# Optimization experiments

Measured on AMD Instinct MI355X. Metric: run time of the kernel, lower is better.

The kernel has to match this reference:

```python
import jax, jax.numpy as jnp
import numpy as np

# ViT-Small config
L, D, H, HD = 12, 384, 6, 64
P, IMG, NCLS = 16, 224, 1000
NPATCH = (IMG // P) ** 2  # 196
GAMMA, MIN_TOKENS, EPS = 0.5, 16, 1e-6
SCALE = HD ** -0.5


def _ln(x, w, b, eps=1e-6):
    mu = jnp.mean(x, axis=-1, keepdims=True)
    var = jnp.var(x, axis=-1, keepdims=True)
    return (x - mu) * jax.lax.rsqrt(var + eps) * w + b


def _qkv_split(xn, w, b):
    # xn: [B, Nt, D] -> q,k,v each [B, H, Nt, HD]
    B, Nt, _ = xn.shape
    qkv = (xn @ w.T + b).reshape(B, Nt, 3, H, HD).transpose(2, 0, 3, 1, 4)
    return qkv[0], qkv[1], qkv[2]


def _vit_forward(x, patch_w, patch_b, cls_token, pos_embed,
                 ln1_w, ln1_b, qkv_w, qkv_b, proj_w, proj_b,
                 ln2_w, ln2_b, fc1_w, fc1_b, fc2_w, fc2_b,
                 norm_w, norm_b, head_w, head_b, keep_schedule=None):
    B = x.shape[0]
    # patch embed: conv stride 16 -> [B, D, 14, 14] -> [B, 196, D]
    xp = jax.lax.conv_general_dilated(x, patch_w, (P, P), 'VALID',
                                      dimension_numbers=('NCHW', 'OIHW', 'NCHW'))
    xp = xp.reshape(B, D, NPATCH).transpose(0, 2, 1) + patch_b
    cls = jnp.broadcast_to(cls_token, (B, 1, D))
    xt = jnp.concatenate([cls, xp], axis=1) + pos_embed  # [B, 197, D]

    N = NPATCH
    prev_mass = jnp.asarray(1.0, jnp.float32)
    schedule = []
    for l in range(L):
        if keep_schedule is not None:
            keep_idx = keep_schedule[l]
        elif N > MIN_TOKENS:
            # CLS-only attention importance scoring (cheap pass)
            xn = _ln(xt, ln1_w[l], ln1_b[l])
            q, k, v = _qkv_split(xn, qkv_w[l], qkv_b[l])
            a_cls = jax.nn.softmax(jnp.einsum('bhqd,bhkd->bhqk', q[:, :, :1], k) * SCALE, axis=-1)[:, :, 0, :]  # [B,H,Nt]
            vnorm = jnp.linalg.norm(v, axis=-1)  # [B,H,Nt]
            imp = (a_cls * vnorm).mean(axis=1)   # [B,Nt]
            imp_p = imp[:, 1:]                   # patch importance
            mass = jnp.mean(imp_p.sum(-1) / (imp.sum(-1) + EPS))
            keep_ratio = float(jnp.clip(GAMMA * mass / (prev_mass + EPS), 0.0, 1.0))
            N_next = max(MIN_TOKENS, int(N * keep_ratio))
            if N_next < N:
                scores = imp_p.mean(0)  # shared keep set across batch (index_select semantics)
                top = jax.lax.top_k(scores, N_next)[1]
                keep_idx = jnp.concatenate([jnp.zeros((1,), jnp.int32),
                                            jnp.sort(top).astype(jnp.int32) + 1])
            else:
                keep_idx = None
            prev_mass = mass
        else:
            keep_idx = None
        schedule.append(keep_idx)
        if keep_idx is not None:
            xt = jnp.take(xt, keep_idx, axis=1)
            N = int(keep_idx.shape[0]) - 1

        # full transformer block on surviving tokens
        Nt = xt.shape[1]
        xn = _ln(xt, ln1_w[l], ln1_b[l])
        q, k, v = _qkv_split(xn, qkv_w[l], qkv_b[l])
        a = jax.nn.softmax(jnp.einsum('bhqd,bhkd->bhqk', q, k) * SCALE, axis=-1)
        o = jnp.einsum('bhqk,bhkd->bhqd', a, v).transpose(0, 2, 1, 3).reshape(B, Nt, D)
        xt = xt + o @ proj_w[l].T + proj_b[l]
        h = _ln(xt, ln2_w[l], ln2_b[l])
        h = jax.nn.gelu(h @ fc1_w[l].T + fc1_b[l], approximate=False)
        xt = xt + h @ fc2_w[l].T + fc2_b[l]

    xt = _ln(xt, norm_w, norm_b)
    logits = xt[:, 0] @ head_w.T + head_b
    return logits, schedule


def setup_inputs() -> dict:
    key = jax.random.key(0)
    ks = jax.random.split(key, 10)
    rn = lambda k, s, sc=0.02: jax.random.normal(k, s, jnp.float32) * sc
    return {
        'x': jax.random.normal(ks[0], (64, 3, IMG, IMG), jnp.float32),
        'patch_w': rn(ks[1], (D, 3, P, P)),
        'patch_b': jnp.zeros((D,), jnp.float32),
        'cls_token': rn(ks[2], (1, 1, D)),
        'pos_embed': rn(ks[3], (1, NPATCH + 1, D)),
        'ln1_w': jnp.ones((L, D), jnp.float32), 'ln1_b': jnp.zeros((L, D), jnp.float32),
        'qkv_w': rn(ks[4], (L, 3 * D, D)), 'qkv_b': jnp.zeros((L, 3 * D), jnp.float32),
        'proj_w': rn(ks[5], (L, D, D)), 'proj_b': jnp.zeros((L, D), jnp.float32),
        'ln2_w': jnp.ones((L, D), jnp.float32), 'ln2_b': jnp.zeros((L, D), jnp.float32),
        'fc1_w': rn(ks[6], (L, 4 * D, D)), 'fc1_b': jnp.zeros((L, 4 * D), jnp.float32),
        'fc2_w': rn(ks[7], (L, D, 4 * D)), 'fc2_b': jnp.zeros((L, D), jnp.float32),
        'norm_w': jnp.ones((D,), jnp.float32), 'norm_b': jnp.zeros((D,), jnp.float32),
        'head_w': rn(ks[8], (NCLS, D)), 'head_b': jnp.zeros((NCLS,), jnp.float32),
    }


def reference(x, patch_w, patch_b, cls_token, pos_embed, ln1_w, ln1_b, qkv_w, qkv_b,
              proj_w, proj_b, ln2_w, ln2_b, fc1_w, fc1_b, fc2_w, fc2_b,
              norm_w, norm_b, head_w, head_b):
    logits, _ = _vit_forward(x, patch_w, patch_b, cls_token, pos_embed, ln1_w, ln1_b,
                             qkv_w, qkv_b, proj_w, proj_b, ln2_w, ln2_b,
                             fc1_w, fc1_b, fc2_w, fc2_b, norm_w, norm_b, head_w, head_b)
    return logits
```

## Files before the change

kernel.cpp:

```cpp
#include <hip/hip_runtime.h>
#include <hip/hip_bf16.h>

static constexpr int kL = 12;
static constexpr int kD = 384;
static constexpr int kH = 6;
static constexpr int kB = 64;
static constexpr int kNP = 196;
static constexpr int kBAND = 197;
static constexpr int kNCLS = 1000;
static constexpr float kSCALE = 0.125f;
static constexpr float kEPS = 1e-6f;
static constexpr size_t kWQ = (size_t)kB * kH * kBAND * 64;
static constexpr int kBH = kB * kH;

typedef __attribute__((ext_vector_type(8))) short short8;
typedef __attribute__((ext_vector_type(4))) float f32x4;

__device__ __forceinline__ float gelu_f(float x) {
    return 0.5f * x * (1.0f + erff(x * 0.70710678118654752440f));
}
__device__ __forceinline__ unsigned short f2bf(float x) {
    __hip_bfloat16 h = __float2bfloat16(x);
    return *(unsigned short*)&h;
}
__device__ __forceinline__ float bf2f(unsigned short u) {
    unsigned int x = ((unsigned int)u) << 16;
    return __uint_as_float(x);
}

__global__ __launch_bounds__(384) void k_init(int* si, float* sf,
                                              const float* __restrict__ cls,
                                              const float* __restrict__ pos,
                                              unsigned short* __restrict__ xtA,
                                              float2* __restrict__ pstats) {
    int b = blockIdx.x, c = threadIdx.x;
    unsigned short hv = f2bf(cls[c] + pos[c]);
    xtA[(size_t)b * kBAND * kD + c] = hv;
    float v = bf2f(hv);
    __shared__ float r1[384], r2[384];
    r1[c] = v; r2[c] = v * v;
    __syncthreads();
    if (c < 128) { r1[c] += r1[c + 128] + r1[c + 256]; r2[c] += r2[c + 128] + r2[c + 256]; }
    __syncthreads();
    for (int st = 64; st; st >>= 1) {
        if (c < st) { r1[c] += r1[c + st]; r2[c] += r2[c + st]; }
        __syncthreads();
    }
    if (c == 0) {
        pstats[(size_t)(b * kBAND) * 8 + 0] = make_float2(r1[0], r2[0]);
#pragma unroll
        for (int nn = 1; nn < 6; ++nn) pstats[(size_t)(b * kBAND) * 8 + nn] = make_float2(0.f, 0.f);
        if (b == 0) { si[0] = kBAND; sf[0] = 1.0f; }
    }
}

__global__ __launch_bounds__(256) void k_cvtall(
    const float* __restrict__ s0, const float* __restrict__ s1, const float* __restrict__ s2,
    const float* __restrict__ s3, const float* __restrict__ s4,
    __hip_bfloat16* __restrict__ d0, __hip_bfloat16* __restrict__ d1, __hip_bfloat16* __restrict__ d2,
    __hip_bfloat16* __restrict__ d3, __hip_bfloat16* __restrict__ d4) {
    const int c0 = 73728, c1 = 1400832, c2 = 1843200, c3 = 3612672, c4 = 5382144;
    int stride = gridDim.x * 256;
    for (int i = blockIdx.x * 256 + threadIdx.x; i < c4; i += stride) {
        const float* src; __hip_bfloat16* dst; int off;
        if (i < c0)      { src = s0; dst = d0; off = i; }
        else if (i < c1) { src = s1; dst = d1; off = i - c0; }
        else if (i < c2) { src = s2; dst = d2; off = i - c1; }
        else if (i < c3) { src = s3; dst = d3; off = i - c2; }
        else             { src = s4; dst = d4; off = i - c3; }
        float4 v = ((const float4*)src)[off];
        dst[4 * off + 0] = __float2bfloat16(v.x);
        dst[4 * off + 1] = __float2bfloat16(v.y);
        dst[4 * off + 2] = __float2bfloat16(v.z);
        dst[4 * off + 3] = __float2bfloat16(v.w);
    }
}

template<int ACT_GELU, int MODE, int LNA, int STATS>
__global__ __launch_bounds__(256) void k_mgemm(
    const void* __restrict__ Av, int lda,
    const unsigned short* __restrict__ W, int K,
    const float* __restrict__ bias,
    unsigned short* __restrict__ Cv, int ldc,
    const void* __restrict__ Rv,
    const int* __restrict__ keepR,
    const float* __restrict__ lnw, const float* __restrict__ lnb,
    int rT, int nT, int band,
    const int* __restrict__ NtPtr, int ntConst,
    const float2* __restrict__ pstatsIn, float2* __restrict__ pstatsOut)
{
    __shared__ __align__(16) unsigned char pool[18432];
    unsigned short (*As)[72] = (unsigned short (*)[72])pool;
    unsigned short (*Ws)[72] = (unsigned short (*)[72])(pool + 9216);
    unsigned short (*Cu)[76] = (unsigned short (*)[76])pool;
    __shared__ float mus[64], rss[64];

    int Nt = NtPtr ? NtPtr[0] : ntConst;
    unsigned int rowsTotal = (unsigned int)kB * (unsigned int)Nt;

    int L = blockIdx.x;
    int xcd = L & 7;
    int m = L >> 3;
    int n = m % nT;
    int r = (m / nT) * 8 + xcd;
    if (r >= rT) return;
    unsigned int r0 = (unsigned int)r * 64;
    int n0 = n * 64;
    if (r0 >= rowsTotal) return;

    const float* Rf = (const float*)Rv;
    const unsigned short* Rb = (const unsigned short*)Rv;

    int tid = threadIdx.x;
    int srow = tid >> 3;
    int scol = (tid & 7) << 3;

    unsigned int rv0 = r0 + srow, rv1 = r0 + srow + 32;
    bool v0 = rv0 < rowsTotal, v1 = rv1 < rowsTotal;
    const unsigned short* ah0 = nullptr; const unsigned short* ah1 = nullptr;
    const float* xb0 = nullptr; const float* xb1 = nullptr;
    if (MODE == 2) {
        if (v0) {
            unsigned int bb = rv0 / (unsigned int)Nt, tt = rv0 - bb * Nt;
            int py = tt / 14, px = tt - py * 14;
            xb0 = (const float*)Av + (size_t)bb * 3 * 224 * 224 + (py * 16) * 224 + px * 16;
        }
        if (v1) {
            unsigned int bb = rv1 / (unsigned int)Nt, tt = rv1 - bb * Nt;
            int py = tt / 14, px = tt - py * 14;
            xb1 = (const float*)Av + (size_t)bb * 3 * 224 * 224 + (py * 16) * 224 + px * 16;
        }
    } else {
        if (v0) {
            unsigned int bb = rv0 / (unsigned int)Nt, tt = rv0 - bb * Nt;
            ah0 = (const unsigned short*)Av + ((size_t)bb * band + tt) * lda;
        }
        if (v1) {
            unsigned int bb = rv1 / (unsigned int)Nt, tt = rv1 - bb * Nt;
            ah1 = (const unsigned short*)Av + ((size_t)bb * band + tt) * lda;
        }
    }
    const unsigned short* wp0 = W + (size_t)(n0 + srow) * K;
    const unsigned short* wp1 = W + (size_t)(n0 + srow + 32) * K;

    float mu0 = 0.f, rs0 = 0.f, mu1 = 0.f, rs1 = 0.f;
    if (LNA) {
        if (tid < 64) {
            unsigned int rv = r0 + tid;
            float mu = 0.f, rsd = 0.f;
            if (rv < rowsTotal) {
                unsigned int bb = rv / (unsigned int)Nt, tt = rv - bb * Nt;
                const float2* ps = pstatsIn + ((size_t)bb * band + tt) * 8;
                float s1 = 0.f, s2 = 0.f;
#pragma unroll
                for (int nn = 0; nn < 6; ++nn) { float2 p = ps[nn]; s1 += p.x; s2 += p.y; }
                mu = s1 * (1.f / 384.f);
                float var = fmaxf(s2 * (1.f / 384.f) - mu * mu, 0.f);
                rsd = rsqrtf(var + kEPS);
            }
            mus[tid] = mu; rss[tid] = rsd;
        }
        __syncthreads();
        mu0 = mus[srow]; rs0 = rss[srow];
        mu1 = mus[srow + 32]; rs1 = rss[srow + 32];
    }

    int wave = tid >> 6, lane = tid & 63;
    int wr32 = ((wave >> 1) & 1) * 32, wc32 = (wave & 1) * 32;
    int l15 = lane & 15, l4 = lane >> 4;

    f32x4 acc00 = {}, acc01 = {}, acc10 = {}, acc11 = {};

    for (int k0 = 0; k0 < K; k0 += 64) {
        uint4 zero = make_uint4(0, 0, 0, 0);
        uint4 a0 = zero, a1 = zero;
        uint4 w0 = *(const uint4*)(wp0 + k0 + scol);
        uint4 w1 = *(const uint4*)(wp1 + k0 + scol);
        if (MODE == 2) {
            int k = k0 + scol;
            int c = k >> 8;
            int rr_ = k & 255;
            int ky = rr_ >> 4, kx = rr_ & 15;
            size_t off = (size_t)c * 50176 + (size_t)ky * 224 + kx;
            if (v0) {
                float4 x0 = *(const float4*)(xb0 + off);
                float4 x1 = *(const float4*)(xb0 + off + 4);
                unsigned short p[8];
                p[0] = f2bf(x0.x); p[1] = f2bf(x0.y); p[2] = f2bf(x0.z); p[3] = f2bf(x0.w);
                p[4] = f2bf(x1.x); p[5] = f2bf(x1.y); p[6] = f2bf(x1.z); p[7] = f2bf(x1.w);
                a0 = *(uint4*)p;
            }
            if (v1) {
                float4 x0 = *(const float4*)(xb1 + off);
                float4 x1 = *(const float4*)(xb1 + off + 4);
                unsigned short p[8];
                p[0] = f2bf(x0.x); p[1] = f2bf(x0.y); p[2] = f2bf(x0.z); p[3] = f2bf(x0.w);
                p[4] = f2bf(x1.x); p[5] = f2bf(x1.y); p[6] = f2bf(x1.z); p[7] = f2bf(x1.w);
                a1 = *(uint4*)p;
            }
        } else if (LNA) {
            float4 lw0 = *(const float4*)(lnw + k0 + scol);
            float4 lw1 = *(const float4*)(lnw + k0 + scol + 4);
            float4 lb0 = *(const float4*)(lnb + k0 + scol);
            float4 lb1 = *(const float4*)(lnb + k0 + scol + 4);
            if (v0) {
                uint4 raw = *(const uint4*)(ah0 + k0 + scol);
                const unsigned short* u = (const unsigned short*)&raw;
                unsigned short p[8];
                p[0] = f2bf((bf2f(u[0]) - mu0) * rs0 * lw0.x + lb0.x);
                p[1] = f2bf((bf2f(u[1]) - mu0) * rs0 * lw0.y + lb0.y);
                p[2] = f2bf((bf2f(u[2]) - mu0) * rs0 * lw0.z + lb0.z);
                p[3] = f2bf((bf2f(u[3]) - mu0) * rs0 * lw0.w + lb0.w);
                p[4] = f2bf((bf2f(u[4]) - mu0) * rs0 * lw1.x + lb1.x);
                p[5] = f2bf((bf2f(u[5]) - mu0) * rs0 * lw1.y + lb1.y);
                p[6] = f2bf((bf2f(u[6]) - mu0) * rs0 * lw1.z + lb1.z);
                p[7] = f2bf((bf2f(u[7]) - mu0) * rs0 * lw1.w + lb1.w);
                a0 = *(uint4*)p;
            }
            if (v1) {
                uint4 raw = *(const uint4*)(ah1 + k0 + scol);
                const unsigned short* u = (const unsigned short*)&raw;
                unsigned short p[8];
                p[0] = f2bf((bf2f(u[0]) - mu1) * rs1 * lw0.x + lb0.x);
                p[1] = f2bf((bf2f(u[1]) - mu1) * rs1 * lw0.y + lb0.y);
                p[2] = f2bf((bf2f(u[2]) - mu1) * rs1 * lw0.z + lb0.z);
                p[3] = f2bf((bf2f(u[3]) - mu1) * rs1 * lw0.w + lb0.w);
                p[4] = f2bf((bf2f(u[4]) - mu1) * rs1 * lw1.x + lb1.x);
                p[5] = f2bf((bf2f(u[5]) - mu1) * rs1 * lw1.y + lb1.y);
                p[6] = f2bf((bf2f(u[6]) - mu1) * rs1 * lw1.z + lb1.z);
                p[7] = f2bf((bf2f(u[7]) - mu1) * rs1 * lw1.w + lb1.w);
                a1 = *(uint4*)p;
            }
        } else {
            a0 = v0 ? *(const uint4*)(ah0 + k0 + scol) : zero;
            a1 = v1 ? *(const uint4*)(ah1 + k0 + scol) : zero;
        }
        __syncthreads();
        *(uint4*)&As[srow][scol] = a0;
        *(uint4*)&As[srow + 32][scol] = a1;
        *(uint4*)&Ws[srow][scol] = w0;
        *(uint4*)&Ws[srow + 32][scol] = w1;
        __syncthreads();
#pragma unroll
        for (int ks = 0; ks < 2; ++ks) {
            short8 af_0 = *(const short8*)&As[wr32 + l15][ks * 32 + l4 * 8];
            short8 af_1 = *(const short8*)&As[wr32 + 16 + l15][ks * 32 + l4 * 8];
            short8 bf_0 = *(const short8*)&Ws[wc32 + l15][ks * 32 + l4 * 8];
            short8 bf_1 = *(const short8*)&Ws[wc32 + 16 + l15][ks * 32 + l4 * 8];
            acc00 = __builtin_amdgcn_mfma_f32_16x16x32_bf16(af_0, bf_0, acc00, 0, 0, 0);
            acc01 = __builtin_amdgcn_mfma_f32_16x16x32_bf16(af_0, bf_1, acc01, 0, 0, 0);
            acc10 = __builtin_amdgcn_mfma_f32_16x16x32_bf16(af_1, bf_0, acc10, 0, 0, 0);
            acc11 = __builtin_amdgcn_mfma_f32_16x16x32_bf16(af_1, bf_1, acc11, 0, 0, 0);
        }
    }

    __syncthreads();
    f32x4 accs[2][2] = { { acc00, acc01 }, { acc10, acc11 } };
#pragma unroll
    for (int fi = 0; fi < 2; ++fi) {
        int lrow = wr32 + fi * 16 + l4 * 4;
        unsigned int rvb = r0 + lrow;
#pragma unroll
        for (int fj = 0; fj < 2; ++fj) {
            int lcol = wc32 + fj * 16 + l15;
            float bv = bias ? bias[n0 + lcol] : 0.f;
#pragma unroll
            for (int rr = 0; rr < 4; ++rr) {
                unsigned int rv = rvb + rr;
                float v = accs[fi][fj][rr] + bv;
                if (ACT_GELU) v = gelu_f(v);
                if (MODE == 2) {
                    if (rv < rowsTotal) {
                        unsigned int bb = rv / (unsigned int)Nt;
                        unsigned int tt = rv - bb * (unsigned int)Nt;
                        v += Rf[(size_t)(tt + 1) * kD + n0 + lcol];
                    }
                } else if (Rv && rv < rowsTotal) {
                    unsigned int bb = rv / (unsigned int)Nt;
                    unsigned int tt = rv - bb * (unsigned int)Nt;
                    size_t rrow = keepR ? ((size_t)bb * band + keepR[tt]) : ((size_t)bb * band + tt);
                    v += bf2f(Rb[rrow * ldc + n0 + lcol]);
                }
                Cu[lrow + rr][lcol] = f2bf(v);
            }
        }
    }
    __syncthreads();

#pragma unroll
    for (int i = 0; i < 2; ++i) {
        int id = tid + (i << 8);
        int row = id >> 3, c2 = id & 7;
        unsigned int rv = r0 + row;
        if (rv < rowsTotal) {
            unsigned int bb = rv / (unsigned int)Nt;
            unsigned int tt = rv - bb * (unsigned int)Nt;
            uint4 val = *(const uint4*)&Cu[row][c2 << 3];
            if (MODE == 1) {
                int which = n0 >= 768 ? 2 : (n0 >= 384 ? 1 : 0);
                int hh = (n0 - which * 384) >> 6;
                *(uint4*)(Cv + (size_t)which * kWQ +
                          (((size_t)bb * kH + hh) * kBAND + tt) * 64 + ((n0 & 63) + (c2 << 3))) = val;
            } else if (MODE == 2) {
                *(uint4*)(Cv + ((size_t)bb * kBAND + tt + 1) * ldc + n0 + (c2 << 3)) = val;
            } else {
                *(uint4*)(Cv + ((size_t)bb * band + tt) * ldc + n0 + (c2 << 3)) = val;
            }
            if (STATS) {
                const unsigned short* u = (const unsigned short*)&val;
                float s1 = 0.f, s2 = 0.f;
#pragma unroll
                for (int e = 0; e < 8; ++e) { float f = bf2f(u[e]); s1 += f; s2 += f * f; }
#pragma unroll
                for (int off = 1; off < 8; off <<= 1) {
                    s1 += __shfl_xor(s1, off, 64);
                    s2 += __shfl_xor(s2, off, 64);
                }
                if (c2 == 0) {
                    size_t sridx = (MODE == 2) ? ((size_t)bb * kBAND + tt + 1)
                                               : ((size_t)bb * band + tt);
                    pstatsOut[sridx * 8 + n] = make_float2(s1, s2);
                }
            }
        }
    }
}

__global__ __launch_bounds__(256) void k_decA(const __hip_bfloat16* __restrict__ qsplit,
                                              float* __restrict__ imph, float* __restrict__ sabh,
                                              const int* __restrict__ si) {
    int Nt = si[0];
    if (Nt - 1 <= 16) return;
    int tid = threadIdx.x, w = tid >> 6, lane = tid & 63;
    int bh = blockIdx.x;
    __shared__ float qs[64];
    __shared__ float sdot[224], svn[224];
    __shared__ float red[256];
    const __hip_bfloat16* qp = qsplit + (size_t)bh * kBAND * 64;
    const __hip_bfloat16* kp = qsplit + kWQ + (size_t)bh * kBAND * 64;
    const __hip_bfloat16* vp = qsplit + 2 * kWQ + (size_t)bh * kBAND * 64;
    if (tid < 64) qs[tid] = __bfloat162float(qp[tid]);
    __syncthreads();
    float qv = qs[lane];
    for (int j = w; j < Nt; j += 8) {
        int j2 = j + 4;
        bool has2 = j2 < Nt;
        float k1 = __bfloat162float(kp[(size_t)j * 64 + lane]);
        float v1 = __bfloat162float(vp[(size_t)j * 64 + lane]);
        float k2 = has2 ? __bfloat162float(kp[(size_t)j2 * 64 + lane]) : 0.f;
        float v2 = has2 ? __bfloat162float(vp[(size_t)j2 * 64 + lane]) : 0.f;
        float p1 = qv * k1, n1 = v1 * v1;
        float p2 = qv * k2, n2 = v2 * v2;
#pragma unroll
        for (int off = 1; off < 64; off <<= 1) {
            p1 += __shfl_xor(p1, off, 64); n1 += __shfl_xor(n1, off, 64);
            p2 += __shfl_xor(p2, off, 64); n2 += __shfl_xor(n2, off, 64);
        }
        if (lane == 0) {
            sdot[j] = p1 * kSCALE; svn[j] = sqrtf(n1);
            if (has2) { sdot[j2] = p2 * kSCALE; svn[j2] = sqrtf(n2); }
        }
    }
    __syncthreads();
    float s = (tid < Nt) ? sdot[tid] : -INFINITY;
    red[tid] = s; __syncthreads();
    for (int st = 128; st; st >>= 1) { if (tid < st) red[tid] = fmaxf(red[tid], red[tid + st]); __syncthreads(); }
    float mmax = red[0]; __syncthreads();
    float e = (tid < Nt) ? expf(s - mmax) : 0.f;
    red[tid] = e; __syncthreads();
    for (int st = 128; st; st >>= 1) { if (tid < st) red[tid] += red[tid + st]; __syncthreads(); }
    float inv = 1.f / red[0];
    float val = (tid < Nt) ? e * inv * svn[tid] : 0.f;
    if (tid < Nt) imph[(size_t)tid * kBH + bh] = val;
    __syncthreads();
    red[tid] = val; __syncthreads();
    for (int st = 128; st; st >>= 1) { if (tid < st) red[tid] += red[tid + st]; __syncthreads(); }
    if (tid == 0) { sabh[2 * bh] = red[0]; sabh[2 * bh + 1] = val; }
}

__global__ __launch_bounds__(256) void k_decB(int* __restrict__ si, float* __restrict__ sf,
                                              const float* __restrict__ imph,
                                              const float* __restrict__ sabh,
                                              int* __restrict__ keep) {
    int Nt = si[0];
    int tid = threadIdx.x;
    if (Nt - 1 <= 16) {
        for (int j = tid; j < Nt; j += 256) keep[j] = j;
        return;
    }
    int N = Nt - 1;
    __shared__ float red[256];
    float v = 0.f;
    if (tid < kB) {
        float sa = 0.f, i0 = 0.f;
#pragma unroll
        for (int hh = 0; hh < kH; ++hh) {
            sa += sabh[2 * (tid * kH + hh)];
            i0 += sabh[2 * (tid * kH + hh) + 1];
        }
        sa *= (1.f / 6.f); i0 *= (1.f / 6.f);
        v = (sa - i0) / (sa + kEPS);
    }
    red[tid] = v; __syncthreads();
    for (int st = 128; st; st >>= 1) { if (tid < st) red[tid] += red[tid + st]; __syncthreads(); }
    float mass = red[0] * (1.f / 64.f);
    float prev = sf[0];
    float ratio = 0.5f * mass / (prev + kEPS);
    ratio = fminf(fmaxf(ratio, 0.f), 1.f);
    int N_next = (int)((double)N * (double)ratio);
    if (N_next < 16) N_next = 16;
    if (tid == 0) sf[0] = mass;
    __syncthreads();
    if (N_next >= N) {
        for (int j = tid; j < Nt; j += 256) keep[j] = j;
        return;
    }
    __shared__ float scq[200][4];
    __shared__ float sc[200];
    __shared__ int flag[200];
    for (int task = tid; task < N * 4; task += 256) {
        int row = task >> 2, seg = task & 3;
        const float4* p = (const float4*)(imph + (size_t)(row + 1) * kBH) + seg * 24;
        float a0 = 0.f, a1 = 0.f, a2 = 0.f, a3 = 0.f;
#pragma unroll
        for (int q = 0; q < 24; q += 4) {
            float4 x0 = p[q + 0], x1 = p[q + 1], x2 = p[q + 2], x3 = p[q + 3];
            a0 += (x0.x + x0.y) + (x0.z + x0.w);
            a1 += (x1.x + x1.y) + (x1.z + x1.w);
            a2 += (x2.x + x2.y) + (x2.z + x2.w);
            a3 += (x3.x + x3.y) + (x3.z + x3.w);
        }
        scq[row][seg] = (a0 + a1) + (a2 + a3);
    }
    __syncthreads();
    if (tid < N) sc[tid] = (scq[tid][0] + scq[tid][1]) + (scq[tid][2] + scq[tid][3]);
    __syncthreads();
    if (tid < N) {
        float s2 = sc[tid];
        int rank = 0;
        for (int i = 0; i < N; ++i) {
            float o2 = sc[i];
            rank += (o2 > s2) || (o2 == s2 && i < tid);
        }
        flag[tid] = (rank < N_next) ? 1 : 0;
    }
    __syncthreads();
    if (tid == 0) {
        keep[0] = 0;
        int pos = 1;
        for (int j = 0; j < N; ++j) if (flag[j]) keep[pos++] = j + 1;
        si[0] = N_next + 1;
    }
}

__global__ __launch_bounds__(256) void k_attn2(const __hip_bfloat16* __restrict__ qsplit,
                                               __hip_bfloat16* __restrict__ o,
                                               const int* __restrict__ si,
                                               const int* __restrict__ keep) {
    __shared__ __align__(16) unsigned short Kb[224][72];
    __shared__ __align__(16) unsigned short Vt[64][228];
    __shared__ __align__(16) unsigned short Pb[4][16][228];
    int Nt = si[0];
    int bh = blockIdx.x;
    int b = bh / kH, h = bh - b * kH;
    int tid = threadIdx.x, w = tid >> 6, lane = tid & 63;
    int l15 = lane & 15, l4 = lane >> 4;
    int nJT = (Nt + 15) >> 4;
    int nKT = (Nt + 31) >> 5;
    int NTP = nKT << 5;

    const unsigned short* qb = (const unsigned short*)qsplit + (size_t)bh * kBAND * 64;
    const unsigned short* kb = (const unsigned short*)qsplit + kWQ + (size_t)bh * kBAND * 64;
    const unsigned short* vb = (const unsigned short*)qsplit + 2 * kWQ + (size_t)bh * kBAND * 64;

    {
        int rr = tid >> 3;
        int c8 = (tid & 7) << 3;
        for (int r = rr; r < NTP; r += 32) {
            uint4 kv = make_uint4(0, 0, 0, 0), vv = make_uint4(0, 0, 0, 0);
            if (r < Nt) {
                int old = keep[r];
                kv = *(const uint4*)(kb + ((size_t)old << 6) + c8);
                vv = *(const uint4*)(vb + ((size_t)old << 6) + c8);
            }
            *(uint4*)&Kb[r][c8] = kv;
            const unsigned short* vs = (const unsigned short*)&vv;
#pragma unroll
            for (int e = 0; e < 8; ++e) Vt[c8 + e][r] = vs[e];
        }
    }
    __syncthreads();

    for (int strip = w; strip < nJT; strip += 4) {
        int tq = (strip << 4) + l15;
        int told = (tq < Nt) ? keep[tq] : 0;
        const unsigned short* qrow = qb + ((size_t)told << 6) + (l4 << 3);
        short8 qf0 = *(const short8*)(qrow);
        short8 qf1 = *(const short8*)(qrow + 32);

        f32x4 sv[13];
#pragma unroll
        for (int jt = 0; jt < 13; ++jt) {
            if (jt < nJT) {
                const unsigned short* kr = &Kb[(jt << 4) + l15][l4 << 3];
                short8 kf0 = *(const short8*)(kr);
                short8 kf1 = *(const short8*)(kr + 32);
                f32x4 a = {};
                a = __builtin_amdgcn_mfma_f32_16x16x32_bf16(qf0, kf0, a, 0, 0, 0);
                a = __builtin_amdgcn_mfma_f32_16x16x32_bf16(qf1, kf1, a, 0, 0, 0);
                sv[jt] = a;
            }
        }
        float mx[4] = { -INFINITY, -INFINITY, -INFINITY, -INFINITY };
#pragma unroll
        for (int jt = 0; jt < 13; ++jt) if (jt < nJT) {
            bool ok = ((jt << 4) + l15) < Nt;
#pragma unroll
            for (int r = 0; r < 4; ++r) {
                float s = ok ? sv[jt][r] * kSCALE : -INFINITY;
                sv[jt][r] = s;
                mx[r] = fmaxf(mx[r], s);
            }
        }
#pragma unroll
        for (int r = 0; r < 4; ++r) {
            mx[r] = fmaxf(mx[r], __shfl_xor(mx[r], 1, 64));
            mx[r] = fmaxf(mx[r], __shfl_xor(mx[r], 2, 64));
            mx[r] = fmaxf(mx[r], __shfl_xor(mx[r], 4, 64));
            mx[r] = fmaxf(mx[r], __shfl_xor(mx[r], 8, 64));
        }
        float sm[4] = { 0.f, 0.f, 0.f, 0.f };
#pragma unroll
        for (int jt = 0; jt < 13; ++jt) if (jt < nJT) {
#pragma unroll
            for (int r = 0; r < 4; ++r) {
                float p = expf(sv[jt][r] - mx[r]);
                sv[jt][r] = p;
                sm[r] += p;
            }
        }
#pragma unroll
        for (int r = 0; r < 4; ++r) {
            sm[r] += __shfl_xor(sm[r], 1, 64);
            sm[r] += __shfl_xor(sm[r], 2, 64);
            sm[r] += __shfl_xor(sm[r], 4, 64);
            sm[r] += __shfl_xor(sm[r], 8, 64);
            sm[r] = 1.f / sm[r];
        }
#pragma unroll
        for (int jt = 0; jt < 13; ++jt) if (jt < nJT) {
#pragma unroll
            for (int r = 0; r < 4; ++r)
                Pb[w][(l4 << 2) + r][(jt << 4) + l15] = f2bf(sv[jt][r] * sm[r]);
        }
        for (int c = (nJT << 4) + lane; c < NTP; c += 64) {
#pragma unroll
            for (int rr2 = 0; rr2 < 16; ++rr2) Pb[w][rr2][c] = 0;
        }
        asm volatile("s_waitcnt lgkmcnt(0)" ::: "memory");
        __builtin_amdgcn_sched_barrier(0);

        f32x4 oacc[4] = { {}, {}, {}, {} };
#pragma unroll
        for (int kt = 0; kt < 7; ++kt) if (kt < nKT) {
            short8 pf = *(const short8*)&Pb[w][l15][(kt << 5) + (l4 << 3)];
#pragma unroll
            for (int dt = 0; dt < 4; ++dt) {
                short8 vf = *(const short8*)&Vt[(dt << 4) + l15][(kt << 5) + (l4 << 3)];
                oacc[dt] = __builtin_amdgcn_mfma_f32_16x16x32_bf16(pf, vf, oacc[dt], 0, 0, 0);
            }
        }
#pragma unroll
        for (int dt = 0; dt < 4; ++dt) {
#pragma unroll
            for (int r = 0; r < 4; ++r) {
                int tqo = (strip << 4) + (l4 << 2) + r;
                if (tqo < Nt)
                    o[((size_t)b * kBAND + tqo) * kD + h * 64 + (dt << 4) + l15] =
                        __float2bfloat16(oacc[dt][r]);
            }
        }
    }
}

__global__ __launch_bounds__(256) void k_head(const unsigned short* __restrict__ X,
                                              const float* __restrict__ nw, const float* __restrict__ nb,
                                              const float* __restrict__ hw, const float* __restrict__ hb,
                                              float* __restrict__ out) {
    int b = blockIdx.x >> 2;
    int tid = threadIdx.x;
    __shared__ float xs[384];
    __shared__ float red[256];
    const unsigned short* row = X + (size_t)b * kBAND * kD;
    float s1 = 0.f, s2 = 0.f;
    for (int c = tid; c < 384; c += 256) { float v = bf2f(row[c]); xs[c] = v; s1 += v; s2 += v * v; }
    red[tid] = s1; __syncthreads();
    for (int st = 128; st; st >>= 1) { if (tid < st) red[tid] += red[tid + st]; __syncthreads(); }
    float sum = red[0]; __syncthreads();
    red[tid] = s2; __syncthreads();
    for (int st = 128; st; st >>= 1) { if (tid < st) red[tid] += red[tid + st]; __syncthreads(); }
    float sq = red[0];
    float mu = sum * (1.f / 384.f);
    float var = fmaxf(sq * (1.f / 384.f) - mu * mu, 0.f);
    float rs = rsqrtf(var + kEPS);
    __syncthreads();
    for (int c = tid; c < 384; c += 256) xs[c] = (xs[c] - mu) * rs * nw[c] + nb[c];
    __syncthreads();
    int n = ((blockIdx.x & 3) << 8) + tid;
    if (n >= kNCLS) return;
    const float* wrow = hw + (size_t)n * kD;
    float acc = 0.f;
#pragma unroll 8
    for (int d = 0; d < kD; d += 4) {
        float4 w4 = *(const float4*)(wrow + d);
        acc += xs[d] * w4.x + xs[d + 1] * w4.y + xs[d + 2] * w4.z + xs[d + 3] * w4.w;
    }
    out[(size_t)b * kNCLS + n] = acc + hb[n];
}

extern "C" void kernel_launch(void* const* d_in, const int* in_sizes, int n_in,
                              void* d_out, int out_size, void* d_ws, size_t ws_size,
                              hipStream_t stream) {
    const float* x       = (const float*)d_in[0];
    const float* patch_w = (const float*)d_in[1];
    const float* patch_b = (const float*)d_in[2];
    const float* cls_tok = (const float*)d_in[3];
    const float* pos     = (const float*)d_in[4];
    const float* ln1w    = (const float*)d_in[5];
    const float* ln1b    = (const float*)d_in[6];
    const float* qkvw    = (const float*)d_in[7];
    const float* qkvb    = (const float*)d_in[8];
    const float* projw   = (const float*)d_in[9];
    const float* projb   = (const float*)d_in[10];
    const float* ln2w    = (const float*)d_in[11];
    const float* ln2b    = (const float*)d_in[12];
    const float* fc1w    = (const float*)d_in[13];
    const float* fc1b    = (const float*)d_in[14];
    const float* fc2w    = (const float*)d_in[15];
    const float* fc2b    = (const float*)d_in[16];
    const float* normw   = (const float*)d_in[17];
    const float* normb   = (const float*)d_in[18];
    const float* headw   = (const float*)d_in[19];
    const float* headb   = (const float*)d_in[20];
    float* out = (float*)d_out;

    char* ws = (char*)d_ws;
    const size_t MB = 1024ull * 1024ull;
    int*   si   = (int*)ws;
    float* sf   = (float*)(ws + 64);
    int*   keep = (int*)(ws + 256);
    float* sabh = (float*)(ws + 4096);
    float* imph = (float*)(ws + 16384);
    unsigned short* xtA = (unsigned short*)(ws + 1 * MB);
    unsigned short* xtB = (unsigned short*)(ws + 12 * MB);
    __hip_bfloat16* obuf = (__hip_bfloat16*)(ws + 23 * MB);
    __hip_bfloat16* qsplit = (__hip_bfloat16*)(ws + 33 * MB);
    __hip_bfloat16* hbuf   = (__hip_bfloat16*)(ws + 33 * MB);
    __hip_bfloat16* wpat = (__hip_bfloat16*)(ws + 110 * MB);
    __hip_bfloat16* wqkv = (__hip_bfloat16*)(ws + 111 * MB);
    __hip_bfloat16* wprj = (__hip_bfloat16*)(ws + 122 * MB);
    __hip_bfloat16* wfc1 = (__hip_bfloat16*)(ws + 126 * MB);
    __hip_bfloat16* wfc2 = (__hip_bfloat16*)(ws + 141 * MB);
    float2* pstats = (float2*)(ws + 156 * MB);

    k_init<<<64, 384, 0, stream>>>(si, sf, cls_tok, pos, xtA, pstats);
    k_cvtall<<<2048, 256, 0, stream>>>(patch_w, qkvw, projw, fc1w, fc2w,
                                       wpat, wqkv, wprj, wfc1, wfc2);

    k_mgemm<0, 2, 0, 1><<<8 * 6 * 25, 256, 0, stream>>>(
        (const void*)x, 768, (const unsigned short*)wpat, 768,
        patch_b, xtA, kD, (const void*)pos, (const int*)nullptr,
        (const float*)nullptr, (const float*)nullptr,
        196, 6, 196, (const int*)nullptr, 196,
        (const float2*)nullptr, pstats);

    unsigned short* cur = xtA; unsigned short* oth = xtB;
    for (int l = 0; l < kL; ++l) {
        const float* l1w = ln1w + l * kD;  const float* l1b = ln1b + l * kD;
        const __hip_bfloat16* qw = wqkv + (size_t)l * 1152 * kD;
        const float* qb = qkvb + l * 1152;
        const __hip_bfloat16* pw = wprj + (size_t)l * kD * kD;
        const float* pb = projb + l * kD;
        const float* l2w = ln2w + l * kD;  const float* l2b = ln2b + l * kD;
        const __hip_bfloat16* f1w = wfc1 + (size_t)l * 1536 * kD;
        const float* f1b = fc1b + l * 1536;
        const __hip_bfloat16* f2w = wfc2 + (size_t)l * kD * 1536;
        const float* f2b = fc2b + l * kD;

        k_mgemm<0, 1, 1, 0><<<8 * 18 * 25, 256, 0, stream>>>(
            (const void*)cur, kD, (const unsigned short*)qw, kD,
            qb, (unsigned short*)qsplit, 1152, (const void*)nullptr, (const int*)nullptr,
            l1w, l1b, 197, 18, kBAND, si, 0,
            (const float2*)pstats, (float2*)nullptr);
        k_decA<<<kB * kH, 256, 0, stream>>>(qsplit, imph, sabh, si);
        k_decB<<<1, 256, 0, stream>>>(si, sf, imph, sabh, keep);
        k_attn2<<<kB * kH, 256, 0, stream>>>(qsplit, obuf, si, keep);
        k_mgemm<0, 0, 0, 1><<<8 * 6 * 25, 256, 0, stream>>>(
            (const void*)obuf, kD, (const unsigned short*)pw, kD,
            pb, oth, kD, (const void*)cur, keep,
            (const float*)nullptr, (const float*)nullptr,
            197, 6, kBAND, si, 0,
            (const float2*)nullptr, pstats);
        { unsigned short* tmp = cur; cur = oth; oth = tmp; }
        k_mgemm<1, 0, 1, 0><<<8 * 24 * 25, 256, 0, stream>>>(
            (const void*)cur, kD, (const unsigned short*)f1w, kD,
            f1b, (unsigned short*)hbuf, 1536, (const void*)nullptr, (const int*)nullptr,
            l2w, l2b, 197, 24, kBAND, si, 0,
            (const float2*)pstats, (float2*)nullptr);
        k_mgemm<0, 0, 0, 1><<<8 * 6 * 25, 256, 0, stream>>>(
            (const void*)hbuf, 1536, (const unsigned short*)f2w, 1536,
            f2b, cur, kD, (const void*)cur, (const int*)nullptr,
            (const float*)nullptr, (const float*)nullptr,
            197, 6, kBAND, si, 0,
            (const float2*)nullptr, pstats);
    }

    k_head<<<kB * 4, 256, 0, stream>>>(cur, normw, normb, headw, headb, out);
}
```

Baseline: 1.191 ms.

## Fold LayerNorm affine into QKV/FC1 weights and apply normalization in epilogue

Folds the LayerNorm gamma into the bf16 QKV and FC1 weights at conversion time, and precomputes per-output-column sums of the folded weights and beta·W. The GEMM then consumes raw bf16 activations and applies the mean/rstd correction in the epilogue, which removes the per-element normalize-and-reconvert work from the A-load path of the LN-fused GEMMs. This adds a setup kernel and changes numerics, since un-normalized activations go through bf16 MMA and the mean is subtracted afterwards, which risks cancellation error.

```diff
diff --git a/kernel.cpp b/kernel.cpp
--- a/kernel.cpp
+++ b/kernel.cpp
@@ -57,23 +57,59 @@
 __global__ __launch_bounds__(256) void k_cvtall(
     const float* __restrict__ s0, const float* __restrict__ s1, const float* __restrict__ s2,
     const float* __restrict__ s3, const float* __restrict__ s4,
+    const float* __restrict__ lw1, const float* __restrict__ lw2,
     __hip_bfloat16* __restrict__ d0, __hip_bfloat16* __restrict__ d1, __hip_bfloat16* __restrict__ d2,
     __hip_bfloat16* __restrict__ d3, __hip_bfloat16* __restrict__ d4) {
     const int c0 = 73728, c1 = 1400832, c2 = 1843200, c3 = 3612672, c4 = 5382144;
     int stride = gridDim.x * 256;
     for (int i = blockIdx.x * 256 + threadIdx.x; i < c4; i += stride) {
-        const float* src; __hip_bfloat16* dst; int off;
+        const float* src; __hip_bfloat16* dst; int off; int fold = 0;
+        const float* lw = nullptr; int perL = 0;
         if (i < c0)      { src = s0; dst = d0; off = i; }
-        else if (i < c1) { src = s1; dst = d1; off = i - c0; }
+        else if (i < c1) { src = s1; dst = d1; off = i - c0; fold = 1; lw = lw1; perL = 442368; }
         else if (i < c2) { src = s2; dst = d2; off = i - c1; }
-        else if (i < c3) { src = s3; dst = d3; off = i - c2; }
+        else if (i < c3) { src = s3; dst = d3; off = i - c2; fold = 1; lw = lw2; perL = 589824; }
         else             { src = s4; dst = d4; off = i - c3; }
         float4 v = ((const float4*)src)[off];
+        if (fold) {
+            int f0 = off << 2;
+            int l = f0 / perL;
+            int k = f0 % 384;
+            float4 g = *(const float4*)(lw + l * 384 + k);
+            v.x *= g.x; v.y *= g.y; v.z *= g.z; v.w *= g.w;
+        }
         dst[4 * off + 0] = __float2bfloat16(v.x);
         dst[4 * off + 1] = __float2bfloat16(v.y);
         dst[4 * off + 2] = __float2bfloat16(v.z);
         dst[4 * off + 3] = __float2bfloat16(v.w);
     }
+}
+
+__global__ __launch_bounds__(256) void k_lncoef(
+    const unsigned short* __restrict__ wq, const float* __restrict__ qkvw_f, const float* __restrict__ ln1b,
+    const unsigned short* __restrict__ wf, const float* __restrict__ fc1w_f, const float* __restrict__ ln2b,
+    float2* __restrict__ qcoef, float2* __restrict__ fcoef) {
+    const int NQ = kL * 1152;
+    const int NF = kL * 1536;
+    int col = blockIdx.x * 4 + (threadIdx.x >> 6);
+    int lane = threadIdx.x & 63;
+    if (col >= NQ + NF) return;
+    bool isQ = col < NQ;
+    int c = isQ ? col : col - NQ;
+    int l = c / (isQ ? 1152 : 1536);
+    const unsigned short* w = (isQ ? wq : wf) + (size_t)c * 384;
+    const float* wo = (isQ ? qkvw_f : fc1w_f) + (size_t)c * 384;
+    const float* lb = (isQ ? ln1b : ln2b) + l * 384;
+    float g = 0.f, bn = 0.f;
+#pragma unroll
+    for (int e = 0; e < 6; ++e) {
+        int k = lane + (e << 6);
+        g += bf2f(w[k]);
+        bn += lb[k] * wo[k];
+    }
+#pragma unroll
+    for (int off = 1; off < 64; off <<= 1) { g += __shfl_xor(g, off, 64); bn += __shfl_xor(bn, off, 64); }
+    if (lane == 0) { if (isQ) qcoef[c] = make_float2(g, bn); else fcoef[c] = make_float2(g, bn); }
 }
 
 template<int ACT_GELU, int MODE, int LNA, int STATS>
@@ -84,7 +120,7 @@
     unsigned short* __restrict__ Cv, int ldc,
     const void* __restrict__ Rv,
     const int* __restrict__ keepR,
-    const float* __restrict__ lnw, const float* __restrict__ lnb,
+    const float2* __restrict__ lncoef,
     int rT, int nT, int band,
     const int* __restrict__ NtPtr, int ntConst,
     const float2* __restrict__ pstatsIn, float2* __restrict__ pstatsOut)
@@ -143,7 +179,6 @@
     const unsigned short* wp0 = W + (size_t)(n0 + srow) * K;
     const unsigned short* wp1 = W + (size_t)(n0 + srow + 32) * K;
 
-    float mu0 = 0.f, rs0 = 0.f, mu1 = 0.f, rs1 = 0.f;
     if (LNA) {
         if (tid < 64) {
             unsigned int rv = r0 + tid;
@@ -161,8 +196,6 @@
             mus[tid] = mu; rss[tid] = rsd;
         }
         __syncthreads();
-        mu0 = mus[srow]; rs0 = rss[srow];
-        mu1 = mus[srow + 32]; rs1 = rss[srow + 32];
     }
 
     int wave = tid >> 6, lane = tid & 63;
@@ -198,39 +231,6 @@
                 p[4] = f2bf(x1.x); p[5] = f2bf(x1.y); p[6] = f2bf(x1.z); p[7] = f2bf(x1.w);
                 a1 = *(uint4*)p;
             }
-        } else if (LNA) {
-            float4 lw0 = *(const float4*)(lnw + k0 + scol);
-            float4 lw1 = *(const float4*)(lnw + k0 + scol + 4);
-            float4 lb0 = *(const float4*)(lnb + k0 + scol);
-            float4 lb1 = *(const float4*)(lnb + k0 + scol + 4);
-            if (v0) {
-                uint4 raw = *(const uint4*)(ah0 + k0 + scol);
-                const unsigned short* u = (const unsigned short*)&raw;
-                unsigned short p[8];
-                p[0] = f2bf((bf2f(u[0]) - mu0) * rs0 * lw0.x + lb0.x);
-                p[1] = f2bf((bf2f(u[1]) - mu0) * rs0 * lw0.y + lb0.y);
-                p[2] = f2bf((bf2f(u[2]) - mu0) * rs0 * lw0.z + lb0.z);
-                p[3] = f2bf((bf2f(u[3]) - mu0) * rs0 * lw0.w + lb0.w);
-                p[4] = f2bf((bf2f(u[4]) - mu0) * rs0 * lw1.x + lb1.x);
-                p[5] = f2bf((bf2f(u[5]) - mu0) * rs0 * lw1.y + lb1.y);
-                p[6] = f2bf((bf2f(u[6]) - mu0) * rs0 * lw1.z + lb1.z);
-                p[7] = f2bf((bf2f(u[7]) - mu0) * rs0 * lw1.w + lb1.w);
-                a0 = *(uint4*)p;
-            }
-            if (v1) {
-                uint4 raw = *(const uint4*)(ah1 + k0 + scol);
-                const unsigned short* u = (const unsigned short*)&raw;
-                unsigned short p[8];
-                p[0] = f2bf((bf2f(u[0]) - mu1) * rs1 * lw0.x + lb0.x);
-                p[1] = f2bf((bf2f(u[1]) - mu1) * rs1 * lw0.y + lb0.y);
-                p[2] = f2bf((bf2f(u[2]) - mu1) * rs1 * lw0.z + lb0.z);
-                p[3] = f2bf((bf2f(u[3]) - mu1) * rs1 * lw0.w + lb0.w);
-                p[4] = f2bf((bf2f(u[4]) - mu1) * rs1 * lw1.x + lb1.x);
-                p[5] = f2bf((bf2f(u[5]) - mu1) * rs1 * lw1.y + lb1.y);
-                p[6] = f2bf((bf2f(u[6]) - mu1) * rs1 * lw1.z + lb1.z);
-                p[7] = f2bf((bf2f(u[7]) - mu1) * rs1 * lw1.w + lb1.w);
-                a1 = *(uint4*)p;
-            }
         } else {
             a0 = v0 ? *(const uint4*)(ah0 + k0 + scol) : zero;
             a1 = v1 ? *(const uint4*)(ah1 + k0 + scol) : zero;
@@ -264,10 +264,18 @@
         for (int fj = 0; fj < 2; ++fj) {
             int lcol = wc32 + fj * 16 + l15;
             float bv = bias ? bias[n0 + lcol] : 0.f;
+            float2 cf = make_float2(0.f, 0.f);
+            if (LNA) cf = lncoef[n0 + lcol];
 #pragma unroll
             for (int rr = 0; rr < 4; ++rr) {
                 unsigned int rv = rvb + rr;
-                float v = accs[fi][fj][rr] + bv;
+                float v;
+                if (LNA) {
+                    float muv = mus[lrow + rr], rsv = rss[lrow + rr];
+                    v = accs[fi][fj][rr] * rsv + bv + cf.y - muv * rsv * cf.x;
+                } else {
+                    v = accs[fi][fj][rr] + bv;
+                }
                 if (ACT_GELU) v = gelu_f(v);
                 if (MODE == 2) {
                     if (rv < rowsTotal) {
@@ -662,26 +670,30 @@
     __hip_bfloat16* wfc1 = (__hip_bfloat16*)(ws + 126 * MB);
     __hip_bfloat16* wfc2 = (__hip_bfloat16*)(ws + 141 * MB);
     float2* pstats = (float2*)(ws + 156 * MB);
+    float2* qcoef  = (float2*)(ws + 158 * MB);
+    float2* fcoef  = (float2*)(ws + 159 * MB);
 
     k_init<<<64, 384, 0, stream>>>(si, sf, cls_tok, pos, xtA, pstats);
     k_cvtall<<<2048, 256, 0, stream>>>(patch_w, qkvw, projw, fc1w, fc2w,
+                                       ln1w, ln2w,
                                        wpat, wqkv, wprj, wfc1, wfc2);
+    k_lncoef<<<8064, 256, 0, stream>>>((const unsigned short*)wqkv, qkvw, ln1b,
+                                       (const unsigned short*)wfc1, fc1w, ln2b,
+                                       qcoef, fcoef);
 
     k_mgemm<0, 2, 0, 1><<<8 * 6 * 25, 256, 0, stream>>>(
         (const void*)x, 768, (const unsigned short*)wpat, 768,
         patch_b, xtA, kD, (const void*)pos, (const int*)nullptr,
-        (const float*)nullptr, (const float*)nullptr,
+        (const float2*)nullptr,
         196, 6, 196, (const int*)nullptr, 196,
         (const float2*)nullptr, pstats);
 
     unsigned short* cur = xtA; unsigned short* oth = xtB;
     for (int l = 0; l < kL; ++l) {
-        const float* l1w = ln1w + l * kD;  const float* l1b = ln1b + l * kD;
         const __hip_bfloat16* qw = wqkv + (size_t)l * 1152 * kD;
         const float* qb = qkvb + l * 1152;
         const __hip_bfloat16* pw = wprj + (size_t)l * kD * kD;
         const float* pb = projb + l * kD;
-        const float* l2w = ln2w + l * kD;  const float* l2b = ln2b + l * kD;
         const __hip_bfloat16* f1w = wfc1 + (size_t)l * 1536 * kD;
         const float* f1b = fc1b + l * 1536;
         const __hip_bfloat16* f2w = wfc2 + (size_t)l * kD * 1536;
@@ -690,7 +702,8 @@
         k_mgemm<0, 1, 1, 0><<<8 * 18 * 25, 256, 0, stream>>>(
             (const void*)cur, kD, (const unsigned short*)qw, kD,
             qb, (unsigned short*)qsplit, 1152, (const void*)nullptr, (const int*)nullptr,
-            l1w, l1b, 197, 18, kBAND, si, 0,
+            (const float2*)(qcoef + (size_t)l * 1152),
+            197, 18, kBAND, si, 0,
             (const float2*)pstats, (float2*)nullptr);
         k_decA<<<kB * kH, 256, 0, stream>>>(qsplit, imph, sabh, si);
         k_decB<<<1, 256, 0, stream>>>(si, sf, imph, sabh, keep);
@@ -698,19 +711,20 @@
         k_mgemm<0, 0, 0, 1><<<8 * 6 * 25, 256, 0, stream>>>(
             (const void*)obuf, kD, (const unsigned short*)pw, kD,
             pb, oth, kD, (const void*)cur, keep,
-            (const float*)nullptr, (const float*)nullptr,
+            (const float2*)nullptr,
             197, 6, kBAND, si, 0,
             (const float2*)nullptr, pstats);
         { unsigned short* tmp = cur; cur = oth; oth = tmp; }
         k_mgemm<1, 0, 1, 0><<<8 * 24 * 25, 256, 0, stream>>>(
             (const void*)cur, kD, (const unsigned short*)f1w, kD,
             f1b, (unsigned short*)hbuf, 1536, (const void*)nullptr, (const int*)nullptr,
-            l2w, l2b, 197, 24, kBAND, si, 0,
+            (const float2*)(fcoef + (size_t)l * 1536),
+            197, 24, kBAND, si, 0,
             (const float2*)pstats, (float2*)nullptr);
         k_mgemm<0, 0, 0, 1><<<8 * 6 * 25, 256, 0, stream>>>(
             (const void*)hbuf, 1536, (const unsigned short*)f2w, 1536,
             f2b, cur, kD, (const void*)cur, (const int*)nullptr,
-            (const float*)nullptr, (const float*)nullptr,
+            (const float2*)nullptr,
             197, 6, kBAND, si, 0,
             (const float2*)nullptr, pstats);
     }
```

After: 1.157 ms. 1.03x faster.
